# Optimization experiments

Hardware: AMD Instinct MI355X
Metric: run time of the kernel (lower is better)

Reference implementation:

```python
import jax, jax.numpy as jnp
import numpy as np
import math

INPUT_SIZE = 512
HIDDEN = 1024
OUTPUT = 512


def _uniform(key, shape, stdv):
    return jax.random.uniform(key, shape, jnp.float32, -stdv, stdv)


def setup_inputs() -> dict:
    key = jax.random.key(0)
    ks = jax.random.split(key, 11)
    stdv = 1.0 / math.sqrt(HIDDEN)
    x = jax.random.normal(ks[0], (128, 512, INPUT_SIZE), jnp.float32)
    return {
        "x": x,
        "w_ih1": _uniform(ks[1], (4 * HIDDEN, INPUT_SIZE), stdv),
        "w_hh1": _uniform(ks[2], (4 * HIDDEN, HIDDEN), stdv),
        "b_ih1": _uniform(ks[3], (4 * HIDDEN,), stdv),
        "b_hh1": _uniform(ks[4], (4 * HIDDEN,), stdv),
        "w_ih2": _uniform(ks[5], (4 * HIDDEN, HIDDEN), stdv),
        "w_hh2": _uniform(ks[6], (4 * HIDDEN, HIDDEN), stdv),
        "b_ih2": _uniform(ks[7], (4 * HIDDEN,), stdv),
        "b_hh2": _uniform(ks[8], (4 * HIDDEN,), stdv),
        "w_out": _uniform(ks[9], (OUTPUT, HIDDEN), 1.0 / math.sqrt(HIDDEN)),
        "b_out": _uniform(ks[10], (OUTPUT,), 1.0 / math.sqrt(HIDDEN)),
    }


def _cell(x_t, h, c, w_ih, w_hh, b_ih, b_hh):
    # gates: [B, 4H], chunk order: i, f, g, o (matches torch chunk(4, 1))
    gates = x_t @ w_ih.T + b_ih + h @ w_hh.T + b_hh
    i, f, g, o = jnp.split(gates, 4, axis=1)
    i = jax.nn.sigmoid(i)
    f = jax.nn.sigmoid(f)
    g = jnp.tanh(g)
    o = jax.nn.sigmoid(o)
    c_new = f * c + i * g
    h_new = o * jnp.tanh(c_new)
    return h_new, c_new


def reference(x, w_ih1, w_hh1, b_ih1, b_hh1, w_ih2, w_hh2, b_ih2, b_hh2, w_out, b_out):
    B = x.shape[0]
    H = w_hh1.shape[1]
    zeros = jnp.zeros((B, H), x.dtype)

    def step(carry, x_t):
        h1, c1, h2, c2 = carry
        h1, c1 = _cell(x_t, h1, c1, w_ih1, w_hh1, b_ih1, b_hh1)
        h2, c2 = _cell(h1, h2, c2, w_ih2, w_hh2, b_ih2, b_hh2)
        return (h1, c1, h2, c2), None

    xs = jnp.swapaxes(x, 0, 1)  # [T, B, D]
    (h1, c1, h2, c2), _ = jax.lax.scan(step, (zeros, zeros, zeros, zeros), xs)
    return h2 @ w_out.T + b_out
```

## Files before the change

kernel.cpp:

```cpp
#include <hip/hip_runtime.h>
#include <hip/hip_bf16.h>
#include <math.h>

typedef __bf16 bf16;
typedef __bf16 bf16x8 __attribute__((ext_vector_type(8)));
typedef float f32x16 __attribute__((ext_vector_type(16)));

#define T_STEPS 512
#define BATCH   128
#define DIN     512
#define HID     1024
#define G4      4096
#define DOUT    512

__device__ __forceinline__ float sigm(float x){ return 1.0f / (1.0f + __expf(-x)); }

__device__ __forceinline__ int zoff(int b, int k){
    return (k >> 5) * 4096 + ((k >> 4) & 1) * 2048 + (b >> 5) * 512 +
           ((k >> 3) & 1) * 256 + (b & 31) * 8 + (k & 7);
}

#define GLOAD_LDS(gsrc, ldsdst) \
  __builtin_amdgcn_global_load_lds((const __attribute__((address_space(1))) void*)(gsrc), \
                                   (__attribute__((address_space(3))) void*)(ldsdst), 16, 0, 0)


__global__ void wstage(const float* __restrict__ src, bf16* __restrict__ hi,
                       bf16* __restrict__ lo, int lk){
    int i = blockIdx.x * 256 + threadIdx.x;
    int K = 1 << lk;
    int n = i >> lk, k = i & (K - 1);
    float v = src[i];
    bf16 h = (bf16)v;
    int off = ((n >> 6) * (K >> 5) + (k >> 5)) * 2048 + ((k >> 4) & 1) * 1024 +
              ((n >> 5) & 1) * 512 + ((k >> 3) & 1) * 256 + (n & 31) * 8 + (k & 7);
    hi[off] = h;
    lo[off] = (bf16)(v - (float)h);
}

__global__ void xstage(const float* __restrict__ x, bf16* __restrict__ hi,
                       bf16* __restrict__ lo){
    int i = blockIdx.x * 256 + threadIdx.x;
    int d = i & 511;
    int b = (i >> 9) & 127;
    int t = i >> 16;
    float v = x[((size_t)b * T_STEPS + t) * DIN + d];
    bf16 h = (bf16)v;
    size_t off = (size_t)t * 65536 + zoff(b, d);
    hi[off] = h;
    lo[off] = (bf16)(v - (float)h);
}

__global__ void bias_kernel(const float* __restrict__ bih1, const float* __restrict__ bhh1,
                            const float* __restrict__ bih2, const float* __restrict__ bhh2,
                            float* __restrict__ bias1, float* __restrict__ bias2){
    int i = blockIdx.x * 256 + threadIdx.x;
    if (i < G4){
        bias1[i] = bih1[i] + bhh1[i];
        bias2[i] = bih2[i] + bhh2[i];
    }
}

__global__ __launch_bounds__(256)
void gemm_step(const bf16* __restrict__ x_h,  const bf16* __restrict__ x_l,
               const bf16* __restrict__ h1_h, const bf16* __restrict__ h1_l,
               const bf16* __restrict__ h2_h, const bf16* __restrict__ h2_l,
               const bf16* __restrict__ w1x_h, const bf16* __restrict__ w1x_l,
               const bf16* __restrict__ w1h_h, const bf16* __restrict__ w1h_l,
               const bf16* __restrict__ w2i_h, const bf16* __restrict__ w2i_l,
               const bf16* __restrict__ w2h_h, const bf16* __restrict__ w2h_l,
               float* __restrict__ gpart, int t)
{
    int g     = blockIdx.x >> 6;
    int ntile = blockIdx.x & 63;
    if (t == T_STEPS && g < 3) return;
    if (t == 0 && g >= 3)      return;
    int p1 = (t - 1) & 1;
    int p2 = t & 1;

    const bf16 *Ah, *Al, *Wh, *Wl;
    int kstep0, wsteps;
    switch (g){
      case 0: Ah = x_h + (size_t)t * 65536; Al = x_l + (size_t)t * 65536;
              Wh = w1x_h; Wl = w1x_l; kstep0 = 0;  wsteps = 16; break;
      case 1: Ah = h1_h + p1 * 131072; Al = h1_l + p1 * 131072;
              Wh = w1h_h; Wl = w1h_l; kstep0 = 0;  wsteps = 32; break;
      case 2: Ah = h1_h + p1 * 131072; Al = h1_l + p1 * 131072;
              Wh = w1h_h; Wl = w1h_l; kstep0 = 16; wsteps = 32; break;
      case 3: Ah = h1_h + p1 * 131072; Al = h1_l + p1 * 131072;
              Wh = w2i_h; Wl = w2i_l; kstep0 = 0;  wsteps = 32; break;
      case 4: Ah = h1_h + p1 * 131072; Al = h1_l + p1 * 131072;
              Wh = w2i_h; Wl = w2i_l; kstep0 = 16; wsteps = 32; break;
      case 5: Ah = h2_h + p2 * 131072; Al = h2_l + p2 * 131072;
              Wh = w2h_h; Wl = w2h_l; kstep0 = 0;  wsteps = 32; break;
      default: Ah = h2_h + p2 * 131072; Al = h2_l + p2 * 131072;
              Wh = w2h_h; Wl = w2h_l; kstep0 = 16; wsteps = 32; break;
    }

    __shared__ __align__(1024) char smem[49152];
    int wave = threadIdx.x >> 6;
    int lane = threadIdx.x & 63;
    int wm = wave >> 1, wn = wave & 1;

    auto stage = [&](int buf, int s){
        int ks = kstep0 + s;
        const bf16* Ash = Ah + (size_t)ks * 4096;
        const bf16* Asl = Al + (size_t)ks * 4096;
        const bf16* Wsh = Wh + ((size_t)ntile * wsteps + ks) * 2048;
        const bf16* Wsl = Wl + ((size_t)ntile * wsteps + ks) * 2048;
        char* base = smem + buf * 24576;
        #pragma unroll
        for (int c = 0; c < 2; ++c){
            int ii = wave * 2 + c;
            GLOAD_LDS(Ash + ii * 512 + lane * 8, base + ii * 1024);
            GLOAD_LDS(Asl + ii * 512 + lane * 8, base + 8192 + ii * 1024);
        }
        GLOAD_LDS(Wsh + wave * 512 + lane * 8, base + 16384 + wave * 1024);
        GLOAD_LDS(Wsl + wave * 512 + lane * 8, base + 20480 + wave * 1024);
    };

    int laneoff = ((lane >> 5) << 9) + ((lane & 31) << 4);
    f32x16 acc0 = {0,0,0,0,0,0,0,0,0,0,0,0,0,0,0,0};
    f32x16 acc1 = {0,0,0,0,0,0,0,0,0,0,0,0,0,0,0,0};

    stage(0, 0);
    __syncthreads();
    for (int s = 0; s < 16; ++s){
        if (s < 15) stage((s + 1) & 1, s + 1);
        const char* b = smem + (s & 1) * 24576;
        #pragma unroll
        for (int k2 = 0; k2 < 2; ++k2){
            bf16x8 a0h = *(const bf16x8*)(b + k2 * 4096 + (wm * 2    ) * 1024 + laneoff);
            bf16x8 a1h = *(const bf16x8*)(b + k2 * 4096 + (wm * 2 + 1) * 1024 + laneoff);
            bf16x8 a0l = *(const bf16x8*)(b + 8192 + k2 * 4096 + (wm * 2    ) * 1024 + laneoff);
            bf16x8 a1l = *(const bf16x8*)(b + 8192 + k2 * 4096 + (wm * 2 + 1) * 1024 + laneoff);
            bf16x8 bh  = *(const bf16x8*)(b + 16384 + k2 * 2048 + wn * 1024 + laneoff);
            bf16x8 bl  = *(const bf16x8*)(b + 20480 + k2 * 2048 + wn * 1024 + laneoff);
            acc0 = __builtin_amdgcn_mfma_f32_32x32x16_bf16(a0h, bh, acc0, 0, 0, 0);
            acc1 = __builtin_amdgcn_mfma_f32_32x32x16_bf16(a1h, bh, acc1, 0, 0, 0);
            acc0 = __builtin_amdgcn_mfma_f32_32x32x16_bf16(a0h, bl, acc0, 0, 0, 0);
            acc1 = __builtin_amdgcn_mfma_f32_32x32x16_bf16(a1h, bl, acc1, 0, 0, 0);
            acc0 = __builtin_amdgcn_mfma_f32_32x32x16_bf16(a0l, bh, acc0, 0, 0, 0);
            acc1 = __builtin_amdgcn_mfma_f32_32x32x16_bf16(a1l, bh, acc1, 0, 0, 0);
        }
        __syncthreads();
    }

    float* gp = gpart + (size_t)g * (BATCH * G4);
    int col = ntile * 64 + wn * 32 + (lane & 31);
    int rbase = 4 * (lane >> 5);
    #pragma unroll
    for (int r = 0; r < 16; ++r){
        int row32 = (r & 3) + 8 * (r >> 2) + rbase;
        gp[(size_t)(wm * 64 + row32) * G4 + col]      = acc0[r];
        gp[(size_t)(wm * 64 + 32 + row32) * G4 + col] = acc1[r];
    }
}

__global__ __launch_bounds__(256)
void cell_step(const float* __restrict__ gpart,
               const float* __restrict__ bias1, const float* __restrict__ bias2,
               float* __restrict__ c1, float* __restrict__ c2,
               bf16* __restrict__ h1_h, bf16* __restrict__ h1_l,
               bf16* __restrict__ h2_h, bf16* __restrict__ h2_l,
               float* __restrict__ h2t, int t)
{
    int tid = blockIdx.x * 256 + threadIdx.x;
    for (int L = 0; L < 2; ++L){
        if (L == 0 && t == T_STEPS) continue;
        if (L == 1 && t == 0)       continue;
        int s = L ? (t - 1) : t;
        int p = s & 1;
        const float* bias = L ? bias2 : bias1;
        float* c  = L ? c2 : c1;
        bf16* hh = (L ? h2_h : h1_h) + p * 131072;
        bf16* hl = (L ? h2_l : h1_l) + p * 131072;
        int sh0 = L ? 3 : 0;
        int nsh = L ? 4 : 3;
        for (int it = tid; it < BATCH * HID; it += 65536){
            int b = it >> 10;
            int j = it & (HID - 1);
            size_t base = (size_t)b * G4 + j;
            float g4[4];
            #pragma unroll
            for (int q = 0; q < 4; ++q){
                float v = bias[j + q * 1024];
                for (int sh = 0; sh < nsh; ++sh)
                    v += gpart[(size_t)(sh0 + sh) * (BATCH * G4) + base + q * 1024];
                g4[q] = v;
            }
            float iv = sigm(g4[0]), fv = sigm(g4[1]), gv = tanhf(g4[2]), ov = sigm(g4[3]);
            float cn = fv * c[it] + iv * gv;
            c[it] = cn;
            float h = ov * tanhf(cn);
            bf16 hb = (bf16)h;
            int off = zoff(b, j);
            hh[off] = hb;
            hl[off] = (bf16)(h - (float)hb);
            if (L == 1 && s == T_STEPS - 1) h2t[(size_t)j * BATCH + b] = h;
        }
    }
}

__global__ __launch_bounds__(128)
void outproj(const float* __restrict__ h2t, const float* __restrict__ wout,
             const float* __restrict__ bout, float* __restrict__ out){
    int o = blockIdx.x;
    int b = threadIdx.x;
    float acc = bout[o];
    const float* wr = wout + (size_t)o * HID;
    for (int k = 0; k < HID; ++k)
        acc += wr[k] * h2t[(size_t)k * BATCH + b];
    out[(size_t)b * DOUT + o] = acc;
}

extern "C" void kernel_launch(void* const* d_in, const int* in_sizes, int n_in,
                              void* d_out, int out_size, void* d_ws, size_t ws_size,
                              hipStream_t stream)
{
    const float* x    = (const float*)d_in[0];
    const float* wih1 = (const float*)d_in[1];
    const float* whh1 = (const float*)d_in[2];
    const float* bih1 = (const float*)d_in[3];
    const float* bhh1 = (const float*)d_in[4];
    const float* wih2 = (const float*)d_in[5];
    const float* whh2 = (const float*)d_in[6];
    const float* bih2 = (const float*)d_in[7];
    const float* bhh2 = (const float*)d_in[8];
    const float* wout = (const float*)d_in[9];
    const float* bout = (const float*)d_in[10];
    float* out = (float*)d_out;

    char* p = (char*)d_ws;
    auto alloc = [&](size_t bytes) -> char* {
        char* r = p;
        p += (bytes + 1023) & ~(size_t)1023;
        return r;
    };

    bf16* x_h   = (bf16*)alloc((size_t)T_STEPS * 65536 * 2);
    bf16* x_l   = (bf16*)alloc((size_t)T_STEPS * 65536 * 2);
    bf16* w1x_h = (bf16*)alloc((size_t)G4 * DIN * 2);
    bf16* w1x_l = (bf16*)alloc((size_t)G4 * DIN * 2);
    bf16* w1h_h = (bf16*)alloc((size_t)G4 * HID * 2);
    bf16* w1h_l = (bf16*)alloc((size_t)G4 * HID * 2);
    bf16* w2i_h = (bf16*)alloc((size_t)G4 * HID * 2);
    bf16* w2i_l = (bf16*)alloc((size_t)G4 * HID * 2);
    bf16* w2h_h = (bf16*)alloc((size_t)G4 * HID * 2);
    bf16* w2h_l = (bf16*)alloc((size_t)G4 * HID * 2);
    float* bias1 = (float*)alloc(G4 * 4);
    float* bias2 = (float*)alloc(G4 * 4);
    char* zbase = p;
    bf16* h1_h = (bf16*)alloc((size_t)2 * 131072 * 2);
    bf16* h1_l = (bf16*)alloc((size_t)2 * 131072 * 2);
    bf16* h2_h = (bf16*)alloc((size_t)2 * 131072 * 2);
    bf16* h2_l = (bf16*)alloc((size_t)2 * 131072 * 2);
    float* c1  = (float*)alloc((size_t)BATCH * HID * 4);
    float* c2  = (float*)alloc((size_t)BATCH * HID * 4);
    size_t zbytes = (size_t)(p - zbase);
    float* gpart = (float*)alloc((size_t)7 * BATCH * G4 * 4);
    float* h2t   = (float*)alloc((size_t)HID * BATCH * 4);
    (void)ws_size; (void)in_sizes; (void)n_in; (void)out_size;

    wstage<<<(G4 * DIN) / 256, 256, 0, stream>>>(wih1, w1x_h, w1x_l, 9);
    wstage<<<(G4 * HID) / 256, 256, 0, stream>>>(whh1, w1h_h, w1h_l, 10);
    wstage<<<(G4 * HID) / 256, 256, 0, stream>>>(wih2, w2i_h, w2i_l, 10);
    wstage<<<(G4 * HID) / 256, 256, 0, stream>>>(whh2, w2h_h, w2h_l, 10);
    bias_kernel<<<(G4 + 255) / 256, 256, 0, stream>>>(bih1, bhh1, bih2, bhh2, bias1, bias2);
    xstage<<<(T_STEPS * BATCH * DIN) / 256, 256, 0, stream>>>(x, x_h, x_l);
    hipMemsetAsync(zbase, 0, zbytes, stream);

    for (int t = 0; t <= T_STEPS; ++t){
        gemm_step<<<448, 256, 0, stream>>>(x_h, x_l, h1_h, h1_l, h2_h, h2_l,
                                           w1x_h, w1x_l, w1h_h, w1h_l,
                                           w2i_h, w2i_l, w2h_h, w2h_l, gpart, t);
        cell_step<<<256, 256, 0, stream>>>(gpart, bias1, bias2, c1, c2,
                                           h1_h, h1_l, h2_h, h2_l, h2t, t);
    }

    outproj<<<DOUT, BATCH, 0, stream>>>(h2t, wout, bout, out);
}
```

Measured before the change: 11.81 ms.

## Widen per-block GEMM N tile from 64 to 128 columns

Each gemm_step block now computes a 128x128 output tile instead of 128x64. The weight staging layout is changed to match, and each wave holds four 32x32 accumulators, which doubles reuse of the A fragments loaded from LDS. The grid shrinks from 448 to 224 blocks, so A-operand traffic per output drops, at the cost of fewer blocks on a 256-CU part, more LDS (64KB) and more registers per block.

```diff
diff --git a/kernel.cpp b/kernel.cpp
--- a/kernel.cpp
+++ b/kernel.cpp
@@ -32,8 +32,8 @@
     int n = i >> lk, k = i & (K - 1);
     float v = src[i];
     bf16 h = (bf16)v;
-    int off = ((n >> 6) * (K >> 5) + (k >> 5)) * 2048 + ((k >> 4) & 1) * 1024 +
-              ((n >> 5) & 1) * 512 + ((k >> 3) & 1) * 256 + (n & 31) * 8 + (k & 7);
+    int off = ((n >> 7) * (K >> 5) + (k >> 5)) * 4096 + ((k >> 4) & 1) * 2048 +
+              ((n >> 5) & 3) * 512 + ((k >> 3) & 1) * 256 + (n & 31) * 8 + (k & 7);
     hi[off] = h;
     lo[off] = (bf16)(v - (float)h);
 }
@@ -71,89 +71,97 @@
                const bf16* __restrict__ w2h_h, const bf16* __restrict__ w2h_l,
                float* __restrict__ gpart, int t)
 {
-    int g     = blockIdx.x >> 6;
-    int ntile = blockIdx.x & 63;
+    int g     = blockIdx.x >> 5;
+    int ntile = blockIdx.x & 31;
     if (t == T_STEPS && g < 3) return;
     if (t == 0 && g >= 3)      return;
-    int p1 = (t - 1) & 1;
-    int p2 = t & 1;
+    int p1 = (t - 1) & 1, p2 = t & 1;
 
     const bf16 *Ah, *Al, *Wh, *Wl;
-    int kstep0, wsteps;
+    int kstep0, wks;
     switch (g){
       case 0: Ah = x_h + (size_t)t * 65536; Al = x_l + (size_t)t * 65536;
-              Wh = w1x_h; Wl = w1x_l; kstep0 = 0;  wsteps = 16; break;
+              Wh = w1x_h; Wl = w1x_l; kstep0 = 0;  wks = 16; break;
       case 1: Ah = h1_h + p1 * 131072; Al = h1_l + p1 * 131072;
-              Wh = w1h_h; Wl = w1h_l; kstep0 = 0;  wsteps = 32; break;
+              Wh = w1h_h; Wl = w1h_l; kstep0 = 0;  wks = 32; break;
       case 2: Ah = h1_h + p1 * 131072; Al = h1_l + p1 * 131072;
-              Wh = w1h_h; Wl = w1h_l; kstep0 = 16; wsteps = 32; break;
+              Wh = w1h_h; Wl = w1h_l; kstep0 = 16; wks = 32; break;
       case 3: Ah = h1_h + p1 * 131072; Al = h1_l + p1 * 131072;
-              Wh = w2i_h; Wl = w2i_l; kstep0 = 0;  wsteps = 32; break;
+              Wh = w2i_h; Wl = w2i_l; kstep0 = 0;  wks = 32; break;
       case 4: Ah = h1_h + p1 * 131072; Al = h1_l + p1 * 131072;
-              Wh = w2i_h; Wl = w2i_l; kstep0 = 16; wsteps = 32; break;
+              Wh = w2i_h; Wl = w2i_l; kstep0 = 16; wks = 32; break;
       case 5: Ah = h2_h + p2 * 131072; Al = h2_l + p2 * 131072;
-              Wh = w2h_h; Wl = w2h_l; kstep0 = 0;  wsteps = 32; break;
+              Wh = w2h_h; Wl = w2h_l; kstep0 = 0;  wks = 32; break;
       default: Ah = h2_h + p2 * 131072; Al = h2_l + p2 * 131072;
-              Wh = w2h_h; Wl = w2h_l; kstep0 = 16; wsteps = 32; break;
-    }
-
-    __shared__ __align__(1024) char smem[49152];
-    int wave = threadIdx.x >> 6;
-    int lane = threadIdx.x & 63;
+              Wh = w2h_h; Wl = w2h_l; kstep0 = 16; wks = 32; break;
+    }
+
+    __shared__ __align__(1024) char smem[65536];
+    int wave = threadIdx.x >> 6, lane = threadIdx.x & 63;
     int wm = wave >> 1, wn = wave & 1;
+    int laneoff = ((lane >> 5) << 9) + ((lane & 31) << 4);
 
     auto stage = [&](int buf, int s){
         int ks = kstep0 + s;
         const bf16* Ash = Ah + (size_t)ks * 4096;
         const bf16* Asl = Al + (size_t)ks * 4096;
-        const bf16* Wsh = Wh + ((size_t)ntile * wsteps + ks) * 2048;
-        const bf16* Wsl = Wl + ((size_t)ntile * wsteps + ks) * 2048;
-        char* base = smem + buf * 24576;
+        const bf16* Wsh = Wh + ((size_t)ntile * wks + ks) * 4096;
+        const bf16* Wsl = Wl + ((size_t)ntile * wks + ks) * 4096;
+        char* base = smem + buf * 32768;
         #pragma unroll
         for (int c = 0; c < 2; ++c){
             int ii = wave * 2 + c;
-            GLOAD_LDS(Ash + ii * 512 + lane * 8, base + ii * 1024);
-            GLOAD_LDS(Asl + ii * 512 + lane * 8, base + 8192 + ii * 1024);
+            GLOAD_LDS(Ash + ii * 512 + lane * 8, base          + ii * 1024);
+            GLOAD_LDS(Asl + ii * 512 + lane * 8, base + 8192   + ii * 1024);
+            GLOAD_LDS(Wsh + ii * 512 + lane * 8, base + 16384  + ii * 1024);
+            GLOAD_LDS(Wsl + ii * 512 + lane * 8, base + 24576  + ii * 1024);
         }
-        GLOAD_LDS(Wsh + wave * 512 + lane * 8, base + 16384 + wave * 1024);
-        GLOAD_LDS(Wsl + wave * 512 + lane * 8, base + 20480 + wave * 1024);
     };
 
-    int laneoff = ((lane >> 5) << 9) + ((lane & 31) << 4);
-    f32x16 acc0 = {0,0,0,0,0,0,0,0,0,0,0,0,0,0,0,0};
-    f32x16 acc1 = {0,0,0,0,0,0,0,0,0,0,0,0,0,0,0,0};
+    f32x16 a00 = {0,0,0,0,0,0,0,0,0,0,0,0,0,0,0,0};
+    f32x16 a01 = a00, a10 = a00, a11 = a00;
 
     stage(0, 0);
     __syncthreads();
     for (int s = 0; s < 16; ++s){
         if (s < 15) stage((s + 1) & 1, s + 1);
-        const char* b = smem + (s & 1) * 24576;
+        const char* b = smem + (s & 1) * 32768;
         #pragma unroll
         for (int k2 = 0; k2 < 2; ++k2){
-            bf16x8 a0h = *(const bf16x8*)(b + k2 * 4096 + (wm * 2    ) * 1024 + laneoff);
-            bf16x8 a1h = *(const bf16x8*)(b + k2 * 4096 + (wm * 2 + 1) * 1024 + laneoff);
-            bf16x8 a0l = *(const bf16x8*)(b + 8192 + k2 * 4096 + (wm * 2    ) * 1024 + laneoff);
-            bf16x8 a1l = *(const bf16x8*)(b + 8192 + k2 * 4096 + (wm * 2 + 1) * 1024 + laneoff);
-            bf16x8 bh  = *(const bf16x8*)(b + 16384 + k2 * 2048 + wn * 1024 + laneoff);
-            bf16x8 bl  = *(const bf16x8*)(b + 20480 + k2 * 2048 + wn * 1024 + laneoff);
-            acc0 = __builtin_amdgcn_mfma_f32_32x32x16_bf16(a0h, bh, acc0, 0, 0, 0);
-            acc1 = __builtin_amdgcn_mfma_f32_32x32x16_bf16(a1h, bh, acc1, 0, 0, 0);
-            acc0 = __builtin_amdgcn_mfma_f32_32x32x16_bf16(a0h, bl, acc0, 0, 0, 0);
-            acc1 = __builtin_amdgcn_mfma_f32_32x32x16_bf16(a1h, bl, acc1, 0, 0, 0);
-            acc0 = __builtin_amdgcn_mfma_f32_32x32x16_bf16(a0l, bh, acc0, 0, 0, 0);
-            acc1 = __builtin_amdgcn_mfma_f32_32x32x16_bf16(a1l, bh, acc1, 0, 0, 0);
+            bf16x8 ah0 = *(const bf16x8*)(b + k2*4096 + (wm*2    )*1024 + laneoff);
+            bf16x8 ah1 = *(const bf16x8*)(b + k2*4096 + (wm*2 + 1)*1024 + laneoff);
+            bf16x8 al0 = *(const bf16x8*)(b + 8192  + k2*4096 + (wm*2    )*1024 + laneoff);
+            bf16x8 al1 = *(const bf16x8*)(b + 8192  + k2*4096 + (wm*2 + 1)*1024 + laneoff);
+            bf16x8 wh0 = *(const bf16x8*)(b + 16384 + k2*4096 + (wn*2    )*1024 + laneoff);
+            bf16x8 wh1 = *(const bf16x8*)(b + 16384 + k2*4096 + (wn*2 + 1)*1024 + laneoff);
+            bf16x8 wl0 = *(const bf16x8*)(b + 24576 + k2*4096 + (wn*2    )*1024 + laneoff);
+            bf16x8 wl1 = *(const bf16x8*)(b + 24576 + k2*4096 + (wn*2 + 1)*1024 + laneoff);
+            a00 = __builtin_amdgcn_mfma_f32_32x32x16_bf16(ah0, wh0, a00, 0, 0, 0);
+            a01 = __builtin_amdgcn_mfma_f32_32x32x16_bf16(ah0, wh1, a01, 0, 0, 0);
+            a10 = __builtin_amdgcn_mfma_f32_32x32x16_bf16(ah1, wh0, a10, 0, 0, 0);
+            a11 = __builtin_amdgcn_mfma_f32_32x32x16_bf16(ah1, wh1, a11, 0, 0, 0);
+            a00 = __builtin_amdgcn_mfma_f32_32x32x16_bf16(ah0, wl0, a00, 0, 0, 0);
+            a01 = __builtin_amdgcn_mfma_f32_32x32x16_bf16(ah0, wl1, a01, 0, 0, 0);
+            a10 = __builtin_amdgcn_mfma_f32_32x32x16_bf16(ah1, wl0, a10, 0, 0, 0);
+            a11 = __builtin_amdgcn_mfma_f32_32x32x16_bf16(ah1, wl1, a11, 0, 0, 0);
+            a00 = __builtin_amdgcn_mfma_f32_32x32x16_bf16(al0, wh0, a00, 0, 0, 0);
+            a01 = __builtin_amdgcn_mfma_f32_32x32x16_bf16(al0, wh1, a01, 0, 0, 0);
+            a10 = __builtin_amdgcn_mfma_f32_32x32x16_bf16(al1, wh0, a10, 0, 0, 0);
+            a11 = __builtin_amdgcn_mfma_f32_32x32x16_bf16(al1, wh1, a11, 0, 0, 0);
         }
         __syncthreads();
     }
 
     float* gp = gpart + (size_t)g * (BATCH * G4);
-    int col = ntile * 64 + wn * 32 + (lane & 31);
-    int rbase = 4 * (lane >> 5);
+    int col0 = ntile * 128 + (wn * 2    ) * 32 + (lane & 31);
+    int col1 = ntile * 128 + (wn * 2 + 1) * 32 + (lane & 31);
     #pragma unroll
     for (int r = 0; r < 16; ++r){
-        int row32 = (r & 3) + 8 * (r >> 2) + rbase;
-        gp[(size_t)(wm * 64 + row32) * G4 + col]      = acc0[r];
-        gp[(size_t)(wm * 64 + 32 + row32) * G4 + col] = acc1[r];
+        int row32 = (r & 3) + 8 * (r >> 2) + 4 * (lane >> 5);
+        gp[(size_t)(wm * 64 + row32) * G4 + col0]      = a00[r];
+        gp[(size_t)(wm * 64 + row32) * G4 + col1]      = a01[r];
+        gp[(size_t)(wm * 64 + 32 + row32) * G4 + col0] = a10[r];
+        gp[(size_t)(wm * 64 + 32 + row32) * G4 + col1] = a11[r];
     }
 }
 
@@ -271,7 +279,7 @@
     hipMemsetAsync(zbase, 0, zbytes, stream);
 
     for (int t = 0; t <= T_STEPS; ++t){
-        gemm_step<<<448, 256, 0, stream>>>(x_h, x_l, h1_h, h1_l, h2_h, h2_l,
+        gemm_step<<<224, 256, 0, stream>>>(x_h, x_l, h1_h, h1_l, h2_h, h2_l,
                                            w1x_h, w1x_l, w1h_h, w1h_l,
                                            w2i_h, w2i_l, w2h_h, w2h_l, gpart, t);
         cell_step<<<256, 256, 0, stream>>>(gpart, bias1, bias2, c1, c2,
```

Result: slower. 13.26 ms (+12.3%).
